# Performance work log

Hardware: AMD Instinct MI355X
Metric: run time of the kernel (lower is better)

## Reference

```python
import jax, jax.numpy as jnp
import numpy as np

D_MODEL = 1024
NUM_HEADS = 16
D_K = D_MODEL // NUM_HEADS


def setup_inputs() -> dict:
    key = jax.random.key(0)
    ks = jax.random.split(key, 5)
    s = 1.0 / np.sqrt(D_MODEL)
    return {
        "x": jax.random.normal(ks[0], (2, 2048, D_MODEL), dtype=jnp.float32),
        "Wq": jax.random.normal(ks[1], (D_MODEL, D_MODEL), dtype=jnp.float32) * s,
        "bq": jnp.zeros((D_MODEL,), dtype=jnp.float32),
        "Wk": jax.random.normal(ks[2], (D_MODEL, D_MODEL), dtype=jnp.float32) * s,
        "bk": jnp.zeros((D_MODEL,), dtype=jnp.float32),
        "Wv": jax.random.normal(ks[3], (D_MODEL, D_MODEL), dtype=jnp.float32) * s,
        "bv": jnp.zeros((D_MODEL,), dtype=jnp.float32),
        "Wo": jax.random.normal(ks[4], (D_MODEL, D_MODEL), dtype=jnp.float32) * s,
        "bo": jnp.zeros((D_MODEL,), dtype=jnp.float32),
    }


def reference(x, Wq, bq, Wk, bk, Wv, bv, Wo, bo):
    B, S, D = x.shape
    H, dk = NUM_HEADS, D_K
    Q = x @ Wq + bq  # [B, S, D]
    K = x @ Wk + bk
    V = x @ Wv + bv
    # Faithful to the torch code: plain .view(B, H, S, dk) (NO transpose),
    # i.e. heads are carved out of the flattened (S*D) dim, not the feature dim.
    Q = Q.reshape(B, H, S, dk)
    K = K.reshape(B, H, S, dk)
    V = V.reshape(B, H, S, dk)
    scores = jnp.einsum("bhqd,bhkd->bhqk", Q, K) / jnp.sqrt(jnp.float32(dk))
    attn = jax.nn.softmax(scores, axis=-1)  # [B, H, S, S]
    ctx = jnp.einsum("bhqk,bhkd->bhqd", attn, V)  # [B, H, S, dk]
    out = ctx.reshape(B, S, D) @ Wo + bo
    return out  # dropout is identity in eval mode
```

## Files before the change

kernel.cpp:

```cpp
#include <hip/hip_runtime.h>
#include <hip/hip_bf16.h>
#include <math.h>

#define D_MODEL 1024
#define SEQ     2048
#define BATCH   2
#define NHEAD   16
#define DKH     64
#define BH      (BATCH * NHEAD)

typedef unsigned short u16;
typedef unsigned int   u32;
typedef __bf16 bf16x8 __attribute__((ext_vector_type(8)));
typedef float  f32x4  __attribute__((ext_vector_type(4)));

#define MFMA16(a, b, c) __builtin_amdgcn_mfma_f32_16x16x32_bf16((a), (b), (c), 0, 0, 0)
#define AS1 __attribute__((address_space(1)))
#define AS3 __attribute__((address_space(3)))

#define QSCALE 0.18033688f

__device__ __forceinline__ u16 f2bf(float x) {
    u32 u = __float_as_uint(x);
    u += 0x7fffu + ((u >> 16) & 1u);
    return (u16)(u >> 16);
}
__device__ __forceinline__ float bf2f(u16 b) {
    return __uint_as_float(((u32)b) << 16);
}
__device__ __forceinline__ void gl16(const u16* g, void* lds) {
    __builtin_amdgcn_global_load_lds((const AS1 u32*)g, (AS3 u32*)lds, 16, 0, 0);
}

__global__ __launch_bounds__(256) void conv_all(
    const float* __restrict__ x, u16* __restrict__ Xh, int n4,
    const float* __restrict__ W0, const float* __restrict__ W1,
    const float* __restrict__ W2, const float* __restrict__ W3,
    u16* __restrict__ H0, u16* __restrict__ L0, u16* __restrict__ H1, u16* __restrict__ L1,
    u16* __restrict__ H2, u16* __restrict__ L2, u16* __restrict__ H3, u16* __restrict__ L3)
{
    const int t = threadIdx.x;
    if ((int)blockIdx.x < 4096) {
        int i = blockIdx.x * 256 + t;
        if (i >= n4) return;
        float4 v = reinterpret_cast<const float4*>(x)[i];
        uint2 H;
        H.x = f2bf(v.x) | ((u32)f2bf(v.y) << 16);
        H.y = f2bf(v.z) | ((u32)f2bf(v.w) << 16);
        reinterpret_cast<uint2*>(Xh)[i] = H;
        return;
    }
    int id = blockIdx.x - 4096;
    int bx = id & 15, by = (id >> 4) & 15, bz = id >> 8;
    const float* W; u16 *Ht, *Lt;
    if (bz == 0)      { W = W0; Ht = H0; Lt = L0; }
    else if (bz == 1) { W = W1; Ht = H1; Lt = L1; }
    else if (bz == 2) { W = W2; Ht = H2; Lt = L2; }
    else              { W = W3; Ht = H3; Lt = L3; }

    __shared__ float T[64][65];
    const int n0 = bx * 64, k0 = by * 64;
    #pragma unroll
    for (int i = 0; i < 4; ++i) {
        int f = t + i * 256;
        int kr = f >> 4, ns = (f & 15) * 4;
        float4 v = *reinterpret_cast<const float4*>(&W[(size_t)(k0 + kr) * D_MODEL + n0 + ns]);
        T[kr][ns + 0] = v.x; T[kr][ns + 1] = v.y; T[kr][ns + 2] = v.z; T[kr][ns + 3] = v.w;
    }
    __syncthreads();
    #pragma unroll
    for (int i = 0; i < 4; ++i) {
        int f = t + i * 256;
        int nr = f >> 4, ks = (f & 15) * 4;
        u16 hh[4], ll[4];
        #pragma unroll
        for (int j = 0; j < 4; ++j) {
            float xv = T[ks + j][nr];
            u16 hb = f2bf(xv);
            hh[j] = hb;
            ll[j] = f2bf(xv - bf2f(hb));
        }
        uint2 H, L;
        H.x = hh[0] | ((u32)hh[1] << 16); H.y = hh[2] | ((u32)hh[3] << 16);
        L.x = ll[0] | ((u32)ll[1] << 16); L.y = ll[2] | ((u32)ll[3] << 16);
        size_t o = (size_t)(n0 + nr) * D_MODEL + k0 + ks;
        *reinterpret_cast<uint2*>(&Ht[o]) = H;
        *reinterpret_cast<uint2*>(&Lt[o]) = L;
    }
}

__global__ __launch_bounds__(512, 2) void gemm_qkv(
    const u16* __restrict__ AhG,
    const u16* __restrict__ Bqh, const u16* __restrict__ Bql,
    const u16* __restrict__ Bkh, const u16* __restrict__ Bkl,
    const u16* __restrict__ Bvh, const u16* __restrict__ Bvl,
    const float* __restrict__ bq, const float* __restrict__ bk, const float* __restrict__ bv,
    u16* __restrict__ Qb, u16* __restrict__ Kb, u16* __restrict__ Vb)
{
    constexpr int K = D_MODEL, N = D_MODEL;
    __shared__ u16 LB[2][28672];

    const int tid  = threadIdx.x;
    const int wv   = tid >> 6;
    const int lane = tid & 63;
    const int quad = lane >> 4;
    const int l16  = lane & 15;
    const int wm   = wv & 1, wn = wv >> 1;
    const int brow = blockIdx.y * 128, bcol = blockIdx.x * 128;

    const u16* sp[7];
    int sldb[7];
    #pragma unroll
    for (int j = 0; j < 7; ++j) {
        int c = (j < 3) ? (wv * 3 + j)
              : (j < 5) ? (24 + wv * 2 + (j - 3))
                        : (40 + wv * 2 + (j - 5));
        int a = c >> 3, cc = c & 7;
        int row = cc * 16 + (lane >> 2);
        int gseg = (lane & 3) ^ ((lane >> 3) & 3);
        const u16* p;
        if (a == 0)      p = AhG;
        else if (a == 1) p = Bqh;
        else if (a == 2) p = Bql;
        else if (a == 3) p = Bkh;
        else if (a == 4) p = Bkl;
        else if (a == 5) p = Bvh;
        else             p = Bvl;
        int rbase = (a == 0) ? brow : bcol;
        sp[j]   = p + (size_t)(rbase + row) * K + gseg * 8;
        sldb[j] = a * 8192 + cc * 1024;
    }

    int aro[4], bro[2];
    #pragma unroll
    for (int i = 0; i < 4; ++i) {
        int mr = wm * 64 + i * 16 + l16;
        aro[i] = mr * 64 + ((quad ^ ((mr >> 1) & 3)) * 16);
    }
    #pragma unroll
    for (int i = 0; i < 2; ++i) {
        int nr = wn * 32 + i * 16 + l16;
        bro[i] = nr * 64 + ((quad ^ ((nr >> 1) & 3)) * 16);
    }

    f32x4 acc[3][4][2] = {};

    auto rdB = [&](int cur, int m, bf16x8 (&bh)[2], bf16x8 (&bl)[2]) {
        const int bbh = (1 + 2 * m) * 8192, bbl = (2 + 2 * m) * 8192;
        #pragma unroll
        for (int i = 0; i < 2; ++i) {
            bh[i] = *reinterpret_cast<const bf16x8*>((const char*)LB[cur] + bbh + bro[i]);
            bl[i] = *reinterpret_cast<const bf16x8*>((const char*)LB[cur] + bbl + bro[i]);
        }
    };
    auto mm = [&](int m, bf16x8 (&ah)[4], bf16x8 (&bh)[2], bf16x8 (&bl)[2]) {
        __builtin_amdgcn_s_setprio(1);
        #pragma unroll
        for (int mi = 0; mi < 4; ++mi)
            #pragma unroll
            for (int ni = 0; ni < 2; ++ni) {
                f32x4 c = acc[m][mi][ni];
                c = MFMA16(ah[mi], bh[ni], c);
                c = MFMA16(ah[mi], bl[ni], c);
                acc[m][mi][ni] = c;
            }
        __builtin_amdgcn_s_setprio(0);
    };

    #pragma unroll
    for (int j = 0; j < 7; ++j)
        gl16(sp[j], (char*)LB[0] + sldb[j]);

    for (int it = 0; it < K / 32 - 1; ++it) {
        const int cur = it & 1, nx = cur ^ 1;
        const int k1 = (it + 1) * 32;
        bf16x8 ah[4], bh[2], bl[2];

        asm volatile("s_waitcnt vmcnt(4)" ::: "memory");
        __builtin_amdgcn_s_barrier();
        #pragma unroll
        for (int i = 0; i < 4; ++i)
            ah[i] = *reinterpret_cast<const bf16x8*>((const char*)LB[cur] + aro[i]);
        rdB(cur, 0, bh, bl);
        gl16(sp[0] + k1, (char*)LB[nx] + sldb[0]);
        gl16(sp[1] + k1, (char*)LB[nx] + sldb[1]);
        gl16(sp[2] + k1, (char*)LB[nx] + sldb[2]);
        mm(0, ah, bh, bl);

        asm volatile("s_waitcnt vmcnt(5)" ::: "memory");
        __builtin_amdgcn_s_barrier();
        rdB(cur, 1, bh, bl);
        gl16(sp[3] + k1, (char*)LB[nx] + sldb[3]);
        gl16(sp[4] + k1, (char*)LB[nx] + sldb[4]);
        mm(1, ah, bh, bl);

        asm volatile("s_waitcnt vmcnt(5)" ::: "memory");
        __builtin_amdgcn_s_barrier();
        rdB(cur, 2, bh, bl);
        gl16(sp[5] + k1, (char*)LB[nx] + sldb[5]);
        gl16(sp[6] + k1, (char*)LB[nx] + sldb[6]);
        mm(2, ah, bh, bl);
    }

    {
        const int cur = (K / 32 - 1) & 1;
        bf16x8 ah[4], bh[2], bl[2];

        asm volatile("s_waitcnt vmcnt(4)" ::: "memory");
        __builtin_amdgcn_s_barrier();
        #pragma unroll
        for (int i = 0; i < 4; ++i)
            ah[i] = *reinterpret_cast<const bf16x8*>((const char*)LB[cur] + aro[i]);
        rdB(cur, 0, bh, bl);
        mm(0, ah, bh, bl);

        asm volatile("s_waitcnt vmcnt(2)" ::: "memory");
        __builtin_amdgcn_s_barrier();
        rdB(cur, 1, bh, bl);
        mm(1, ah, bh, bl);

        asm volatile("s_waitcnt vmcnt(0)" ::: "memory");
        __builtin_amdgcn_s_barrier();
        rdB(cur, 2, bh, bl);
        mm(2, ah, bh, bl);
    }

    #pragma unroll
    for (int m = 0; m < 3; ++m) {
        const float* bias = (m == 0) ? bq : (m == 1) ? bk : bv;
        u16* out = (m == 0) ? Qb : (m == 1) ? Kb : Vb;
        const float sc = (m == 0) ? QSCALE : 1.0f;
        #pragma unroll
        for (int mi = 0; mi < 4; ++mi) {
            #pragma unroll
            for (int ni = 0; ni < 2; ++ni) {
                int col = bcol + wn * 32 + ni * 16 + l16;
                float bvv = bias[col];
                #pragma unroll
                for (int r = 0; r < 4; ++r) {
                    int row = brow + wm * 64 + mi * 16 + quad * 4 + r;
                    out[(size_t)row * N + col] = f2bf((acc[m][mi][ni][r] + bvv) * sc);
                }
            }
        }
    }
}

__global__ __launch_bounds__(512, 2) void gemm_oproj(
    const u16* __restrict__ AhG, const u16* __restrict__ Bh, const u16* __restrict__ Bl,
    const float* __restrict__ bias, float* __restrict__ Cf)
{
    constexpr int K = D_MODEL, N = D_MODEL;
    __shared__ u16 LB[2][12288];

    const int tid  = threadIdx.x;
    const int wv   = tid >> 6;
    const int lane = tid & 63;
    const int quad = lane >> 4;
    const int l16  = lane & 15;
    const int wm   = wv & 1, wn = wv >> 1;
    const int brow = blockIdx.y * 128, bcol = blockIdx.x * 128;

    const u16* sp[3];
    int sldb[3];
    {
        int row  = wv * 16 + (lane >> 2);
        int gseg = (lane & 3) ^ ((lane >> 3) & 3);
        sp[0]   = AhG + (size_t)(brow + row) * K + gseg * 8;
        sp[1]   = Bh  + (size_t)(bcol + row) * K + gseg * 8;
        sp[2]   = Bl  + (size_t)(bcol + row) * K + gseg * 8;
        sldb[0] = wv * 1024;
        sldb[1] = 8192 + wv * 1024;
        sldb[2] = 16384 + wv * 1024;
    }

    int aro[4], bro[2];
    #pragma unroll
    for (int i = 0; i < 4; ++i) {
        int mr = wm * 64 + i * 16 + l16;
        aro[i] = mr * 64 + ((quad ^ ((mr >> 1) & 3)) * 16);
    }
    #pragma unroll
    for (int i = 0; i < 2; ++i) {
        int nr = wn * 32 + i * 16 + l16;
        bro[i] = nr * 64 + ((quad ^ ((nr >> 1) & 3)) * 16);
    }

    f32x4 acc[4][2] = {};

    auto mmc = [&](bf16x8 (&ah)[4], bf16x8 b0, bf16x8 b1) {
        __builtin_amdgcn_s_setprio(1);
        #pragma unroll
        for (int mi = 0; mi < 4; ++mi) {
            f32x4 c0 = acc[mi][0], c1 = acc[mi][1];
            c0 = MFMA16(ah[mi], b0, c0);
            c1 = MFMA16(ah[mi], b1, c1);
            acc[mi][0] = c0; acc[mi][1] = c1;
        }
        __builtin_amdgcn_s_setprio(0);
    };

    #pragma unroll
    for (int j = 0; j < 3; ++j)
        gl16(sp[j], (char*)LB[0] + sldb[j]);

    for (int it = 0; it < K / 32 - 1; ++it) {
        const int cur = it & 1, nx = cur ^ 1;
        const int k1 = (it + 1) * 32;
        bf16x8 ah[4], b0, b1;

        asm volatile("s_waitcnt vmcnt(1)" ::: "memory");
        __builtin_amdgcn_s_barrier();
        #pragma unroll
        for (int i = 0; i < 4; ++i)
            ah[i] = *reinterpret_cast<const bf16x8*>((const char*)LB[cur] + aro[i]);
        b0 = *reinterpret_cast<const bf16x8*>((const char*)LB[cur] + 8192 + bro[0]);
        b1 = *reinterpret_cast<const bf16x8*>((const char*)LB[cur] + 8192 + bro[1]);
        gl16(sp[0] + k1, (char*)LB[nx] + sldb[0]);
        gl16(sp[1] + k1, (char*)LB[nx] + sldb[1]);
        mmc(ah, b0, b1);

        asm volatile("s_waitcnt vmcnt(2)" ::: "memory");
        __builtin_amdgcn_s_barrier();
        b0 = *reinterpret_cast<const bf16x8*>((const char*)LB[cur] + 16384 + bro[0]);
        b1 = *reinterpret_cast<const bf16x8*>((const char*)LB[cur] + 16384 + bro[1]);
        gl16(sp[2] + k1, (char*)LB[nx] + sldb[2]);
        mmc(ah, b0, b1);
    }

    {
        const int cur = (K / 32 - 1) & 1;
        bf16x8 ah[4], b0, b1;

        asm volatile("s_waitcnt vmcnt(1)" ::: "memory");
        __builtin_amdgcn_s_barrier();
        #pragma unroll
        for (int i = 0; i < 4; ++i)
            ah[i] = *reinterpret_cast<const bf16x8*>((const char*)LB[cur] + aro[i]);
        b0 = *reinterpret_cast<const bf16x8*>((const char*)LB[cur] + 8192 + bro[0]);
        b1 = *reinterpret_cast<const bf16x8*>((const char*)LB[cur] + 8192 + bro[1]);
        mmc(ah, b0, b1);

        asm volatile("s_waitcnt vmcnt(0)" ::: "memory");
        __builtin_amdgcn_s_barrier();
        b0 = *reinterpret_cast<const bf16x8*>((const char*)LB[cur] + 16384 + bro[0]);
        b1 = *reinterpret_cast<const bf16x8*>((const char*)LB[cur] + 16384 + bro[1]);
        mmc(ah, b0, b1);
    }

    #pragma unroll
    for (int mi = 0; mi < 4; ++mi) {
        #pragma unroll
        for (int ni = 0; ni < 2; ++ni) {
            int col = bcol + wn * 32 + ni * 16 + l16;
            float bvv = bias[col];
            #pragma unroll
            for (int r = 0; r < 4; ++r) {
                int row = brow + wm * 64 + mi * 16 + quad * 4 + r;
                Cf[(size_t)row * N + col] = acc[mi][ni][r] + bvv;
            }
        }
    }
}

__global__ __launch_bounds__(256) void v_transpose(
    const u16* __restrict__ V, u16* __restrict__ Vt)
{
    __shared__ u16 T[64][72];
    const int bh = blockIdx.y, st = blockIdx.x;
    const u16* src = V + ((size_t)bh * SEQ + (size_t)st * 64) * 64;
    const int t = threadIdx.x;
    #pragma unroll
    for (int i = 0; i < 2; ++i) {
        int c  = t + i * 256;
        int s  = c >> 3;
        int d0 = (c & 7) * 8;
        uint4 v = reinterpret_cast<const uint4*>(src)[c];
        u16 e[8];
        e[0] = (u16)(v.x & 0xffff); e[1] = (u16)(v.x >> 16);
        e[2] = (u16)(v.y & 0xffff); e[3] = (u16)(v.y >> 16);
        e[4] = (u16)(v.z & 0xffff); e[5] = (u16)(v.z >> 16);
        e[6] = (u16)(v.w & 0xffff); e[7] = (u16)(v.w >> 16);
        #pragma unroll
        for (int j = 0; j < 8; ++j) T[d0 + j][s] = e[j];
    }
    __syncthreads();
    const int d = t >> 2, seg = t & 3;
    u16* dst = Vt + (size_t)bh * 64 * SEQ + (size_t)d * SEQ + st * 64;
    #pragma unroll
    for (int gg = 0; gg < 2; ++gg) {
        int g = seg * 2 + gg;
        u32 r0 = *reinterpret_cast<const u32*>(&T[d][2 * g]);
        u32 r1 = *reinterpret_cast<const u32*>(&T[d][2 * g + 16]);
        u32 r2 = *reinterpret_cast<const u32*>(&T[d][2 * g + 32]);
        u32 r3 = *reinterpret_cast<const u32*>(&T[d][2 * g + 48]);
        uint4 w;
        w.x = (r0 & 0xffffu) | (r1 << 16);
        w.y = (r2 & 0xffffu) | (r3 << 16);
        w.z = (r0 >> 16) | (r1 & 0xffff0000u);
        w.w = (r2 >> 16) | (r3 & 0xffff0000u);
        *reinterpret_cast<uint4*>(&dst[8 * g]) = w;
    }
}

__global__ __launch_bounds__(512, 4) void attn_mfma(
    const u16* __restrict__ Qb_g, const u16* __restrict__ Kb_g,
    const u16* __restrict__ Vt_g, u16* __restrict__ Ch_g)
{
    __shared__ u16 KVS[3][8192];
    __shared__ u16 Pb [128 * 72];

    const int tid  = threadIdx.x;
    const int wv   = tid >> 6;
    const int lane = tid & 63;
    const int quad = lane >> 4;
    const int l16  = lane & 15;
    const int id   = blockIdx.x;
    const int bh   = id & 31;
    const int qt   = id >> 5;
    const int qrow = wv * 16;

    const size_t qbase = ((size_t)bh * SEQ + (size_t)qt * 128) * 64;
    const size_t kbh   = (size_t)bh * SEQ * 64;
    const size_t vtbh  = (size_t)bh * 64 * SEQ;

    bf16x8 qf[2];
    #pragma unroll
    for (int ks = 0; ks < 2; ++ks) {
        size_t o = qbase + (size_t)(qrow + l16) * 64 + ks * 32 + quad * 8;
        qf[ks] = *reinterpret_cast<const bf16x8*>(Qb_g + o);
    }

    const u16* sp[2];
    size_t sstep[2];
    int sldb[2];
    #pragma unroll
    for (int j = 0; j < 2; ++j) {
        int c   = wv * 2 + j;
        int arr = c >> 3, cc = c & 7;
        int row = cc * 8 + (lane >> 3);
        int sg  = (lane & 7) ^ (row & 7);
        if (arr == 0) { sp[j] = Kb_g + kbh + (size_t)row * 64 + sg * 8;   sstep[j] = 4096; }
        else          { sp[j] = Vt_g + vtbh + (size_t)row * SEQ + sg * 8; sstep[j] = 64; }
        sldb[j] = arr * 8192 + cc * 1024;
    }

    int fro[4][2];
    #pragma unroll
    for (int t = 0; t < 4; ++t)
        #pragma unroll
        for (int ks = 0; ks < 2; ++ks)
            fro[t][ks] = (t * 16 + l16) * 128 + (((ks * 4 + quad) ^ (l16 & 7)) * 16);

    bf16x8 onesv;
    #pragma unroll
    for (int i = 0; i < 8; ++i) onesv[i] = (__bf16)1.0f;

    f32x4 oacc[4] = {};
    f32x4 lsum = {};

    auto S_step = [&](int bufidx, f32x4 (&sacc)[4]) {
        const char* kb = (const char*)KVS[bufidx];
        #pragma unroll
        for (int t4 = 0; t4 < 4; ++t4) {
            bf16x8 kh0 = *reinterpret_cast<const bf16x8*>(kb + fro[t4][0]);
            bf16x8 kh1 = *reinterpret_cast<const bf16x8*>(kb + fro[t4][1]);
            f32x4 a = sacc[t4];
            a = MFMA16(qf[0], kh0, a);
            a = MFMA16(qf[1], kh1, a);
            sacc[t4] = a;
        }
    };

    auto PV_step = [&](int bufidx) {
        const char* vb = (const char*)KVS[bufidx] + 8192;
        bf16x8 bvf[4][2];
        #pragma unroll
        for (int dt = 0; dt < 4; ++dt) {
            bvf[dt][0] = *reinterpret_cast<const bf16x8*>(vb + fro[dt][0]);
            bvf[dt][1] = *reinterpret_cast<const bf16x8*>(vb + fro[dt][1]);
        }
        bf16x8 ap[2];
        #pragma unroll
        for (int ks = 0; ks < 2; ++ks)
            ap[ks] = *reinterpret_cast<const bf16x8*>(
                &Pb[(qrow + l16) * 72 + ks * 32 + quad * 8]);
        #pragma unroll
        for (int dt = 0; dt < 4; ++dt) {
            oacc[dt] = MFMA16(ap[0], bvf[dt][0], oacc[dt]);
            oacc[dt] = MFMA16(ap[1], bvf[dt][1], oacc[dt]);
        }
        lsum = MFMA16(ap[0], onesv, lsum);
        lsum = MFMA16(ap[1], onesv, lsum);
    };

    auto EXP2_step = [&](f32x4 (&sacc)[4]) {
        const int rowb = qrow + quad * 4;
        #pragma unroll
        for (int r = 0; r < 4; ++r) {
            u32 u0 = __float_as_uint(__builtin_amdgcn_exp2f(sacc[0][r]));
            u32 u1 = __float_as_uint(__builtin_amdgcn_exp2f(sacc[1][r]));
            u32 u2 = __float_as_uint(__builtin_amdgcn_exp2f(sacc[2][r]));
            u32 u3 = __float_as_uint(__builtin_amdgcn_exp2f(sacc[3][r]));
            uint2 w;
            w.x = (u0 >> 16) | (u1 & 0xffff0000u);
            w.y = (u2 >> 16) | (u3 & 0xffff0000u);
            *reinterpret_cast<uint2*>(&Pb[(rowb + r) * 72 + l16 * 4]) = w;
        }
    };

    #pragma unroll
    for (int j = 0; j < 2; ++j)
        gl16(sp[j], (char*)KVS[0] + sldb[j]);

    {
        __syncthreads();
        #pragma unroll
        for (int j = 0; j < 2; ++j)
            gl16(sp[j] + sstep[j], (char*)KVS[1] + sldb[j]);
        f32x4 sacc[4] = {};
        __builtin_amdgcn_s_setprio(1);
        S_step(0, sacc);
        __builtin_amdgcn_s_setprio(0);
        EXP2_step(sacc);
    }

    int cur = 1, prv = 0, nxt = 2;
    for (int kt = 1; kt < SEQ / 64; ++kt) {
        __syncthreads();
        if (kt + 1 < SEQ / 64) {
            #pragma unroll
            for (int j = 0; j < 2; ++j)
                gl16(sp[j] + (size_t)(kt + 1) * sstep[j], (char*)KVS[nxt] + sldb[j]);
        }

        f32x4 sacc[4] = {};
        __builtin_amdgcn_s_setprio(1);
        S_step(cur, sacc);
        PV_step(prv);
        __builtin_amdgcn_s_setprio(0);
        EXP2_step(sacc);

        prv = cur; cur = nxt; nxt = (nxt == 2) ? 0 : nxt + 1;
    }

    __builtin_amdgcn_s_setprio(1);
    PV_step(prv);
    __builtin_amdgcn_s_setprio(0);

    u16* Oh = Ch_g + qbase;
    float inv[4];
    #pragma unroll
    for (int r = 0; r < 4; ++r) inv[r] = 1.0f / lsum[r];
    #pragma unroll
    for (int dt = 0; dt < 4; ++dt)
        #pragma unroll
        for (int r = 0; r < 4; ++r) {
            int row = qrow + quad * 4 + r;
            Oh[(size_t)row * 64 + dt * 16 + l16] = f2bf(oacc[dt][r] * inv[r]);
        }
}

extern "C" void kernel_launch(void* const* d_in, const int* in_sizes, int n_in,
                              void* d_out, int out_size, void* d_ws, size_t ws_size,
                              hipStream_t stream)
{
    const float* x  = (const float*)d_in[0];
    const float* Wq = (const float*)d_in[1];
    const float* bq = (const float*)d_in[2];
    const float* Wk = (const float*)d_in[3];
    const float* bk = (const float*)d_in[4];
    const float* Wv = (const float*)d_in[5];
    const float* bv = (const float*)d_in[6];
    const float* Wo = (const float*)d_in[7];
    const float* bo = (const float*)d_in[8];
    float* out = (float*)d_out;

    const int M = BATCH * SEQ;
    const int N = D_MODEL;
    const size_t NE = (size_t)M * N;
    const size_t NW = (size_t)N * N;

    u16* w16 = (u16*)d_ws;
    u16* Xh   = w16;
    u16* Qb   = Xh   + NE;
    u16* Kb   = Qb   + NE;
    u16* Vb   = Kb   + NE;
    u16* Vtb  = Vb   + NE;
    u16* Ctxh = Vtb  + NE;
    u16* WTqh = Ctxh + NE;
    u16* WTql = WTqh + NW;
    u16* WTkh = WTql + NW;
    u16* WTkl = WTkh + NW;
    u16* WTvh = WTkl + NW;
    u16* WTvl = WTvh + NW;
    u16* WToh = WTvl + NW;
    u16* WTol = WToh + NW;

    conv_all<<<dim3(4096 + 1024), dim3(256), 0, stream>>>(
        x, Xh, (int)(NE / 4),
        Wq, Wk, Wv, Wo, WTqh, WTql, WTkh, WTkl, WTvh, WTvl, WToh, WTol);

    gemm_qkv<<<dim3(N / 128, M / 128), dim3(512), 0, stream>>>(
        Xh, WTqh, WTql, WTkh, WTkl, WTvh, WTvl, bq, bk, bv, Qb, Kb, Vb);

    v_transpose<<<dim3(SEQ / 64, BH), dim3(256), 0, stream>>>(Vb, Vtb);

    attn_mfma<<<dim3((SEQ / 128) * BH), dim3(512), 0, stream>>>(Qb, Kb, Vtb, Ctxh);

    gemm_oproj<<<dim3(N / 128, M / 128), dim3(512), 0, stream>>>(
        Ctxh, WToh, WTol, bo, out);
}
```

Before: 208.6 us.

## Halve GEMM block tiles to 128x64 with 256 threads for more blocks

Both the QKV and output projection GEMMs move from 128x128 tiles with 8 waves to 128x64 tiles with 4 waves. The grid doubles along N and the LDS buffers shrink, so the load assignments and waitcnt values are rebalanced to match. The aim is more blocks to fill the CUs (M=4096, N=1024 gives only 256 blocks before) and lower LDS use per block. The cost is more redundant reads of the A tile and less reuse per block.

```diff
diff --git a/kernel.cpp b/kernel.cpp
--- a/kernel.cpp
+++ b/kernel.cpp
@@ -89,7 +89,7 @@
     }
 }
 
-__global__ __launch_bounds__(512, 2) void gemm_qkv(
+__global__ __launch_bounds__(256, 2) void gemm_qkv(
     const u16* __restrict__ AhG,
     const u16* __restrict__ Bqh, const u16* __restrict__ Bql,
     const u16* __restrict__ Bkh, const u16* __restrict__ Bkl,
@@ -98,7 +98,7 @@
     u16* __restrict__ Qb, u16* __restrict__ Kb, u16* __restrict__ Vb)
 {
     constexpr int K = D_MODEL, N = D_MODEL;
-    __shared__ u16 LB[2][28672];
+    __shared__ u16 LB[2][16384];
 
     const int tid  = threadIdx.x;
     const int wv   = tid >> 6;
@@ -106,29 +106,31 @@
     const int quad = lane >> 4;
     const int l16  = lane & 15;
     const int wm   = wv & 1, wn = wv >> 1;
-    const int brow = blockIdx.y * 128, bcol = blockIdx.x * 128;
-
-    const u16* sp[7];
-    int sldb[7];
-    #pragma unroll
-    for (int j = 0; j < 7; ++j) {
-        int c = (j < 3) ? (wv * 3 + j)
-              : (j < 5) ? (24 + wv * 2 + (j - 3))
-                        : (40 + wv * 2 + (j - 5));
-        int a = c >> 3, cc = c & 7;
-        int row = cc * 16 + (lane >> 2);
+    const int brow = blockIdx.y * 128, bcol = blockIdx.x * 64;
+
+    const u16* ptrs[7] = { AhG, Bqh, Bql, Bkh, Bkl, Bvh, Bvl };
+    const int abase[7] = { 0, 8192, 12288, 16384, 20480, 24576, 28672 };
+    const u16* sp[8];
+    int sldb[8];
+    #pragma unroll
+    for (int j = 0; j < 8; ++j) {
+        int a, cc;
+        if (j < 4) {
+            int c = wv * 4 + j;
+            if (c < 8) { a = 0; cc = c; }
+            else       { a = (c < 12) ? 1 : 2; cc = c & 3; }
+        } else if (j < 6) {
+            int c = wv * 2 + (j - 4);
+            a = 3 + (c >> 2); cc = c & 3;
+        } else {
+            int c = wv * 2 + (j - 6);
+            a = 5 + (c >> 2); cc = c & 3;
+        }
+        int row  = cc * 16 + (lane >> 2);
         int gseg = (lane & 3) ^ ((lane >> 3) & 3);
-        const u16* p;
-        if (a == 0)      p = AhG;
-        else if (a == 1) p = Bqh;
-        else if (a == 2) p = Bql;
-        else if (a == 3) p = Bkh;
-        else if (a == 4) p = Bkl;
-        else if (a == 5) p = Bvh;
-        else             p = Bvl;
         int rbase = (a == 0) ? brow : bcol;
-        sp[j]   = p + (size_t)(rbase + row) * K + gseg * 8;
-        sldb[j] = a * 8192 + cc * 1024;
+        sp[j]   = ptrs[a] + (size_t)(rbase + row) * K + gseg * 8;
+        sldb[j] = abase[a] + cc * 1024;
     }
 
     int aro[4], bro[2];
@@ -146,7 +148,7 @@
     f32x4 acc[3][4][2] = {};
 
     auto rdB = [&](int cur, int m, bf16x8 (&bh)[2], bf16x8 (&bl)[2]) {
-        const int bbh = (1 + 2 * m) * 8192, bbl = (2 + 2 * m) * 8192;
+        const int bbh = abase[1 + 2 * m], bbl = abase[2 + 2 * m];
         #pragma unroll
         for (int i = 0; i < 2; ++i) {
             bh[i] = *reinterpret_cast<const bf16x8*>((const char*)LB[cur] + bbh + bro[i]);
@@ -168,7 +170,7 @@
     };
 
     #pragma unroll
-    for (int j = 0; j < 7; ++j)
+    for (int j = 0; j < 8; ++j)
         gl16(sp[j], (char*)LB[0] + sldb[j]);
 
     for (int it = 0; it < K / 32 - 1; ++it) {
@@ -185,20 +187,21 @@
         gl16(sp[0] + k1, (char*)LB[nx] + sldb[0]);
         gl16(sp[1] + k1, (char*)LB[nx] + sldb[1]);
         gl16(sp[2] + k1, (char*)LB[nx] + sldb[2]);
+        gl16(sp[3] + k1, (char*)LB[nx] + sldb[3]);
         mm(0, ah, bh, bl);
 
-        asm volatile("s_waitcnt vmcnt(5)" ::: "memory");
+        asm volatile("s_waitcnt vmcnt(6)" ::: "memory");
         __builtin_amdgcn_s_barrier();
         rdB(cur, 1, bh, bl);
-        gl16(sp[3] + k1, (char*)LB[nx] + sldb[3]);
         gl16(sp[4] + k1, (char*)LB[nx] + sldb[4]);
+        gl16(sp[5] + k1, (char*)LB[nx] + sldb[5]);
         mm(1, ah, bh, bl);
 
-        asm volatile("s_waitcnt vmcnt(5)" ::: "memory");
+        asm volatile("s_waitcnt vmcnt(6)" ::: "memory");
         __builtin_amdgcn_s_barrier();
         rdB(cur, 2, bh, bl);
-        gl16(sp[5] + k1, (char*)LB[nx] + sldb[5]);
         gl16(sp[6] + k1, (char*)LB[nx] + sldb[6]);
+        gl16(sp[7] + k1, (char*)LB[nx] + sldb[7]);
         mm(2, ah, bh, bl);
     }
 
@@ -246,12 +249,12 @@
     }
 }
 
-__global__ __launch_bounds__(512, 2) void gemm_oproj(
+__global__ __launch_bounds__(256, 2) void gemm_oproj(
     const u16* __restrict__ AhG, const u16* __restrict__ Bh, const u16* __restrict__ Bl,
     const float* __restrict__ bias, float* __restrict__ Cf)
 {
     constexpr int K = D_MODEL, N = D_MODEL;
-    __shared__ u16 LB[2][12288];
+    __shared__ u16 LB[2][8192];
 
     const int tid  = threadIdx.x;
     const int wv   = tid >> 6;
@@ -259,19 +262,22 @@
     const int quad = lane >> 4;
     const int l16  = lane & 15;
     const int wm   = wv & 1, wn = wv >> 1;
-    const int brow = blockIdx.y * 128, bcol = blockIdx.x * 128;
-
-    const u16* sp[3];
-    int sldb[3];
-    {
-        int row  = wv * 16 + (lane >> 2);
+    const int brow = blockIdx.y * 128, bcol = blockIdx.x * 64;
+
+    const u16* ptrs[3] = { AhG, Bh, Bl };
+    const int abase[3] = { 0, 8192, 12288 };
+    const u16* sp[4];
+    int sldb[4];
+    #pragma unroll
+    for (int j = 0; j < 4; ++j) {
+        int a, cc;
+        if (j < 3) { int c = wv * 3 + j;  a = (c < 8) ? 0 : 1; cc = (c < 8) ? c : (c - 8); }
+        else       { a = 2; cc = wv; }
+        int row  = cc * 16 + (lane >> 2);
         int gseg = (lane & 3) ^ ((lane >> 3) & 3);
-        sp[0]   = AhG + (size_t)(brow + row) * K + gseg * 8;
-        sp[1]   = Bh  + (size_t)(bcol + row) * K + gseg * 8;
-        sp[2]   = Bl  + (size_t)(bcol + row) * K + gseg * 8;
-        sldb[0] = wv * 1024;
-        sldb[1] = 8192 + wv * 1024;
-        sldb[2] = 16384 + wv * 1024;
+        int rbase = (a == 0) ? brow : bcol;
+        sp[j]   = ptrs[a] + (size_t)(rbase + row) * K + gseg * 8;
+        sldb[j] = abase[a] + cc * 1024;
     }
 
     int aro[4], bro[2];
@@ -301,7 +307,7 @@
     };
 
     #pragma unroll
-    for (int j = 0; j < 3; ++j)
+    for (int j = 0; j < 4; ++j)
         gl16(sp[j], (char*)LB[0] + sldb[j]);
 
     for (int it = 0; it < K / 32 - 1; ++it) {
@@ -318,13 +324,14 @@
         b1 = *reinterpret_cast<const bf16x8*>((const char*)LB[cur] + 8192 + bro[1]);
         gl16(sp[0] + k1, (char*)LB[nx] + sldb[0]);
         gl16(sp[1] + k1, (char*)LB[nx] + sldb[1]);
+        gl16(sp[2] + k1, (char*)LB[nx] + sldb[2]);
         mmc(ah, b0, b1);
 
-        asm volatile("s_waitcnt vmcnt(2)" ::: "memory");
-        __builtin_amdgcn_s_barrier();
-        b0 = *reinterpret_cast<const bf16x8*>((const char*)LB[cur] + 16384 + bro[0]);
-        b1 = *reinterpret_cast<const bf16x8*>((const char*)LB[cur] + 16384 + bro[1]);
-        gl16(sp[2] + k1, (char*)LB[nx] + sldb[2]);
+        asm volatile("s_waitcnt vmcnt(3)" ::: "memory");
+        __builtin_amdgcn_s_barrier();
+        b0 = *reinterpret_cast<const bf16x8*>((const char*)LB[cur] + 12288 + bro[0]);
+        b1 = *reinterpret_cast<const bf16x8*>((const char*)LB[cur] + 12288 + bro[1]);
+        gl16(sp[3] + k1, (char*)LB[nx] + sldb[3]);
         mmc(ah, b0, b1);
     }
 
@@ -343,8 +350,8 @@
 
         asm volatile("s_waitcnt vmcnt(0)" ::: "memory");
         __builtin_amdgcn_s_barrier();
-        b0 = *reinterpret_cast<const bf16x8*>((const char*)LB[cur] + 16384 + bro[0]);
-        b1 = *reinterpret_cast<const bf16x8*>((const char*)LB[cur] + 16384 + bro[1]);
+        b0 = *reinterpret_cast<const bf16x8*>((const char*)LB[cur] + 12288 + bro[0]);
+        b1 = *reinterpret_cast<const bf16x8*>((const char*)LB[cur] + 12288 + bro[1]);
         mmc(ah, b0, b1);
     }
 
@@ -601,13 +608,13 @@
         x, Xh, (int)(NE / 4),
         Wq, Wk, Wv, Wo, WTqh, WTql, WTkh, WTkl, WTvh, WTvl, WToh, WTol);
 
-    gemm_qkv<<<dim3(N / 128, M / 128), dim3(512), 0, stream>>>(
+    gemm_qkv<<<dim3(N / 64, M / 128), dim3(256), 0, stream>>>(
         Xh, WTqh, WTql, WTkh, WTkl, WTvh, WTvl, bq, bk, bv, Qb, Kb, Vb);
 
     v_transpose<<<dim3(SEQ / 64, BH), dim3(256), 0, stream>>>(Vb, Vtb);
 
     attn_mfma<<<dim3((SEQ / 128) * BH), dim3(512), 0, stream>>>(Qb, Kb, Vtb, Ctxh);
 
-    gemm_oproj<<<dim3(N / 128, M / 128), dim3(512), 0, stream>>>(
+    gemm_oproj<<<dim3(N / 64, M / 128), dim3(256), 0, stream>>>(
         Ctxh, WToh, WTol, bo, out);
 }
```

After: 208.5 us. Within noise of the previous version (-0.1%).
